# Kernel optimization log

Hardware: AMD Instinct MI355X
Metric: run time of the kernel (lower is better)

The kernel has to match this reference:

```python
import jax, jax.numpy as jnp
import numpy as np

NEG_INF = -1e8  # matches neg_inf in the torch source


def setup_inputs() -> dict:
    key = jax.random.key(0)
    k1, k2 = jax.random.split(key)
    N, M = 2048, 2048
    theta = jax.random.normal(k1, (N, M, 3), dtype=jnp.float32)
    A = jax.random.normal(k2, (3, 3), dtype=jnp.float32)
    return {"theta": theta, "A": A}


def _viterbi_forward(theta, A):
    # Softmax-smoothed Viterbi (Needleman-Wunsch-style) DP.
    # States: m=0, x=1, y=2.
    # V[i,j,m] = theta[i-1,j-1,m] + lse(V[i-1,j-1] + A[m])
    # V[i,j,x] = theta[i-1,j-1,x] + lse(V[i-1,j]   + A[x])
    # V[i,j,y] = theta[i-1,j-1,y] + lse(V[i,j-1]   + A[y])
    N, M, _ = theta.shape
    dt = theta.dtype
    ninf = jnp.asarray(NEG_INF, dt)
    Am, Ax, Ay = A[0], A[1], A[2]

    # Row 0 of V (columns 0..M): V[0,0]=[0,-inf,-inf], rest -inf.
    row0 = jnp.full((M + 1, 3), NEG_INF, dtype=dt).at[0, 0].set(0.0)

    def row_step(prev_row, theta_row):
        # prev_row: (M+1, 3) = V[i-1, 0..M]; theta_row: (M, 3) = theta[i-1]
        # m and x states depend only on the previous row -> vectorized over j.
        vm = jax.nn.logsumexp(prev_row[:-1] + Am, axis=-1) + theta_row[:, 0]  # (M,) j=1..M
        vx = jax.nn.logsumexp(prev_row[1:] + Ax, axis=-1) + theta_row[:, 1]   # (M,)
        # y state has a same-row recurrence over j -> scan over columns.
        vm_prev = jnp.concatenate([ninf[None], vm[:-1]])  # V[i, j-1, m]
        vx_prev = jnp.concatenate([ninf[None], vx[:-1]])  # V[i, j-1, x]

        def col_step(vy_prev, inputs):
            vmp, vxp, th_y = inputs
            vy = jax.nn.logsumexp(jnp.stack([vmp, vxp, vy_prev]) + Ay) + th_y
            return vy, vy

        _, vy = jax.lax.scan(col_step, ninf, (vm_prev, vx_prev, theta_row[:, 2]))
        new_row = jnp.concatenate(
            [jnp.full((1, 3), NEG_INF, dtype=dt),  # V[i, 0] = -inf
             jnp.stack([vm, vx, vy], axis=-1)], axis=0)
        return new_row, None

    last_row, _ = jax.lax.scan(row_step, row0, theta)
    # Terminal: Vt = lse(V[N, M])
    return jax.nn.logsumexp(last_row[M])


def reference(theta, A):
    return _viterbi_forward(theta, A)
```

## Files before the change

kernel.cpp:

```cpp
#include <hip/hip_runtime.h>

#define NDIM  2048
#define WAVES 32
#define BCOLS 2176
#define SLOTS 2128
#define ENCB  0x40000000
#define SENTV 0xFFFFFFFFFFFFFFFFull

typedef unsigned long long u64;

__device__ __align__(16) float4 g_S4[(size_t)WAVES * SLOTS * 64];
__device__ __align__(16) u64    g_B[(size_t)(WAVES+1) * BCOLS * 2];

__device__ __forceinline__ u64 ald(const u64* p) {
  return __hip_atomic_load(p, __ATOMIC_RELAXED, __HIP_MEMORY_SCOPE_AGENT);
}
__device__ __forceinline__ void ast(u64* p, u64 v) {
  __hip_atomic_store(p, v, __ATOMIC_RELAXED, __HIP_MEMORY_SCOPE_AGENT);
}
__device__ __forceinline__ float shup1(float x) {
  int v = __builtin_amdgcn_update_dpp(0, __float_as_int(x), 0x138, 0xf, 0xf, false);
  return __int_as_float(v);
}
__device__ __forceinline__ int imax(int a, int b) { return a > b ? a : b; }

__global__ void vit_prep_theta(const float* __restrict__ theta) {
  const int tid = blockIdx.x * blockDim.x + threadIdx.x;
  const int stride = gridDim.x * blockDim.x;
  const int total = WAVES * SLOTS * 64;
  for (int i = tid; i < total; i += stride) {
    const int l    = i & 63;
    const int rest = i >> 6;
    const int s    = rest % SLOTS;
    const int w    = rest / SLOTS;
    const int row  = w * 64 + l;
    const int col  = s - l;
    float4 r = make_float4(0.f, 0.f, 0.f, 0.f);
    if (col >= 0 && col < NDIM) {
      const float* tp = theta + ((size_t)row * NDIM + col) * 3;
      r.x = __expf(tp[0]); r.y = __expf(tp[1]); r.z = __expf(tp[2]);
    }
    g_S4[i] = r;
  }
}

__global__ void vit_prep_bnd() {
  const int tid = blockIdx.x * blockDim.x + threadIdx.x;
  const int stride = gridDim.x * blockDim.x;
  const int nb = (WAVES+1) * BCOLS;
  const u64 hi0 = ((u64)(unsigned)ENCB) << 32;
  for (int i = tid; i < nb; i += stride) {
    int w = i / BCOLS;
    int c = i - w * BCOLS;
    u64 lo, hi;
    if (c > NDIM)    { lo = 0ull; hi = hi0; }
    else if (w == 0) { lo = (c == 0) ? (u64)__float_as_uint(1.0f) : 0ull; hi = hi0; }
    else if (c == 0) { lo = 0ull; hi = hi0; }
    else             { lo = SENTV; hi = SENTV; }
    ast(&g_B[(size_t)i*2],   lo);
    ast(&g_B[(size_t)i*2+1], hi);
  }
}

__global__ void __launch_bounds__(64, 1)
__attribute__((amdgpu_waves_per_eu(1, 1)))
vit_main(const float* __restrict__ A, float* __restrict__ out) {
  const int lane = threadIdx.x;
  const int w    = blockIdx.x;
  const bool isL0 = (lane == 0);
  const int lsel = lane & 15;

  const float a00 = __expf(A[0]), a01 = __expf(A[1]), a02 = __expf(A[2]);
  const float a10 = __expf(A[3]), a11 = __expf(A[4]), a12 = __expf(A[5]);
  const float a20 = __expf(A[6]), a21 = __expf(A[7]), a22 = __expf(A[8]);

  const float4* tb4 = g_S4 + (size_t)w * SLOTS * 64 + lane;
  u64* bin  = g_B + (size_t)w     * BCOLS * 2;
  u64* bout = g_B + (size_t)(w+1) * BCOLS * 2;

  float Mp=0.f,Xp=0.f,Yp=0.f, Mu=0.f,Xu=0.f,Yu=0.f, Mud=0.f,Xud=0.f,Yud=0.f;
  int e_w = 0;

  float4 Ta0  = tb4[0*64],  Ta1  = tb4[1*64],  Ta2  = tb4[2*64],  Ta3  = tb4[3*64];
  float4 Ta4  = tb4[4*64],  Ta5  = tb4[5*64],  Ta6  = tb4[6*64],  Ta7  = tb4[7*64];
  float4 Ta8  = tb4[8*64],  Ta9  = tb4[9*64],  Ta10 = tb4[10*64], Ta11 = tb4[11*64];
  float4 Ta12 = tb4[12*64], Ta13 = tb4[13*64], Ta14 = tb4[14*64], Ta15 = tb4[15*64];
  float4 Tb0  = make_float4(0,0,0,0), Tb1  = Tb0, Tb2  = Tb0, Tb3  = Tb0;
  float4 Tb4  = Tb0, Tb5  = Tb0, Tb6  = Tb0, Tb7  = Tb0;
  float4 Tb8  = Tb0, Tb9  = Tb0, Tb10 = Tb0, Tb11 = Tb0;
  float4 Tb12 = Tb0, Tb13 = Tb0, Tb14 = Tb0, Tb15 = Tb0;

  u64 cLoa, cHia, cLob = 0, cHib = 0;
  u64* rpn;
  {
    u64* rp0 = bin + (size_t)(2 + lsel) * 2;
    cLoa = ald(rp0); cHia = ald(rp0 + 1);
    rpn = rp0 + 32;
  }

  {
    u64 lo = ald(bin), hi = ald(bin + 1);
    while (lo == SENTV || hi == SENTV) { __builtin_amdgcn_s_sleep(2); lo = ald(bin); hi = ald(bin+1); }
    if (isL0) {
      Mud = __uint_as_float((unsigned)lo);
      Xud = __uint_as_float((unsigned)(lo >> 32));
      Yud = __uint_as_float((unsigned)hi);
    }
  }
  {
    u64 lo = ald(bin + 2), hi = ald(bin + 3);
    while (lo == SENTV || hi == SENTV) { __builtin_amdgcn_s_sleep(8); lo = ald(bin+2); hi = ald(bin+3); }
    int ep = (int)((unsigned)(hi >> 32) - (unsigned)ENCB);
    int dd = ep - e_w;
    if (__builtin_amdgcn_readfirstlane(dd) > 48) { e_w = ep; dd = 0; }
    if (isL0) {
      Mu = ldexpf(__uint_as_float((unsigned)lo), dd);
      Xu = ldexpf(__uint_as_float((unsigned)(lo >> 32)), dd);
      Yu = ldexpf(__uint_as_float((unsigned)hi), dd);
    }
  }

#define STEP(U, S, SM, TM)                                                     \
  {                                                                            \
    const int s = base + (U) + 1;            \
    float mn = T##S##U.x * fmaf(a02, Yud, fmaf(a01, Xud, a00*Mud));            \
    float xn = T##S##U.y * fmaf(a12, Yu,  fmaf(a11, Xu,  a10*Mu));             \
    float yn = T##S##U.z * fmaf(a22, Yp,  fmaf(a21, Xp,  a20*Mp));             \
    if ((SM) ? (lane == 63) : (s >= 64 && lane == 63)) {                       \
      u64 slo = ((u64)__float_as_uint(xn) << 32) | __float_as_uint(mn);        \
      u64 shi = ((u64)(unsigned)(e_w + ENCB) << 32) | __float_as_uint(yn);     \
      ast(bO + (size_t)(U)*2,     slo);                                        \
      ast(bO + (size_t)(U)*2 + 1, shi);                                        \
    }                                                                          \
    if ((TM) && s == 2111 && w == 31 && lane == 63) {                          \
      out[0] = (log2f(mn + xn + yn) + (float)e_w) * 0.69314718055994531f;      \
    }                                                                          \
        \
    const float rM = __int_as_float(__builtin_amdgcn_readlane(__float_as_int(Mbf), (U))); \
    const float rX = __int_as_float(__builtin_amdgcn_readlane(__float_as_int(Xbf), (U))); \
    const float rY = __int_as_float(__builtin_amdgcn_readlane(__float_as_int(Ybf), (U))); \
                                                                   \
    Mud = Mu; Xud = Xu; Yud = Yu;                                              \
    const float sm = shup1(mn);                                                \
    const float sx = shup1(xn);                                                \
    const float sy = shup1(yn);                                                \
    Mu = isL0 ? rM : sm;                                                       \
    Xu = isL0 ? rX : sx;                                                       \
    Yu = isL0 ? rY : sy;                                                       \
    Mp = mn; Xp = xn; Yp = yn;                                                 \
  }

#define BLOCK(S, SN, SM, TM)                                                   \
  {                                                                            \
              \
    u64* rpc_ = rpn - 32;                                                      \
    bool bad_ = (cLo##S == SENTV) || (cHi##S == SENTV);                        \
    while (__ballot(bad_)) {                                                   \
      __builtin_amdgcn_s_sleep(1);                                             \
      cLo##S = ald(rpc_); cHi##S = ald(rpc_ + 1);                              \
      bad_ = (cLo##S == SENTV) || (cHi##S == SENTV);                           \
    }                                                                          \
                   \
    {                                                                          \
      const float4* tn_ = tb4 + (size_t)(base + 16) * 64;                      \
      T##SN##0  = tn_[0*64];  T##SN##1  = tn_[1*64];                           \
      T##SN##2  = tn_[2*64];  T##SN##3  = tn_[3*64];                           \
      T##SN##4  = tn_[4*64];  T##SN##5  = tn_[5*64];                           \
      T##SN##6  = tn_[6*64];  T##SN##7  = tn_[7*64];                           \
      T##SN##8  = tn_[8*64];  T##SN##9  = tn_[9*64];                           \
      T##SN##10 = tn_[10*64]; T##SN##11 = tn_[11*64];                          \
      T##SN##12 = tn_[12*64]; T##SN##13 = tn_[13*64];                          \
      T##SN##14 = tn_[14*64]; T##SN##15 = tn_[15*64];                          \
    }                                                                          \
    cLo##SN = ald(rpn); cHi##SN = ald(rpn + 1);                                \
    rpn += 32;                                                                 \
       \
    int dsl = ((int)(unsigned)(cHi##S >> 32) - ENCB) - e_w;                    \
    int dm = dsl;                                                              \
    dm = imax(dm, __shfl_xor(dm, 1));                                          \
    dm = imax(dm, __shfl_xor(dm, 2));                                          \
    dm = imax(dm, __shfl_xor(dm, 4));                                          \
    dm = imax(dm, __shfl_xor(dm, 8));       \
    if (dm > 0) {                                                              \
      const int sh = -dm;                                                      \
      Mp = ldexpf(Mp,sh); Xp = ldexpf(Xp,sh); Yp = ldexpf(Yp,sh);              \
      Mu = ldexpf(Mu,sh); Xu = ldexpf(Xu,sh); Yu = ldexpf(Yu,sh);              \
      Mud= ldexpf(Mud,sh);Xud= ldexpf(Xud,sh);Yud= ldexpf(Yud,sh);             \
      e_w += dm; dsl -= dm;                                                    \
    }                                                                          \
    const float Mbf = ldexpf(__uint_as_float((unsigned)cLo##S), dsl);          \
    const float Xbf = ldexpf(__uint_as_float((unsigned)(cLo##S >> 32)), dsl);  \
    const float Ybf = ldexpf(__uint_as_float((unsigned)cHi##S), dsl);          \
    __builtin_amdgcn_sched_barrier(0);                                         \
                                                       \
    u64* bO = bout + (size_t)(base - 62) * 2;                                  \
    STEP(0,S,SM,TM)  STEP(1,S,SM,TM)  STEP(2,S,SM,TM)  STEP(3,S,SM,TM)         \
    STEP(4,S,SM,TM)  STEP(5,S,SM,TM)  STEP(6,S,SM,TM)  STEP(7,S,SM,TM)         \
    STEP(8,S,SM,TM)  STEP(9,S,SM,TM)  STEP(10,S,SM,TM) STEP(11,S,SM,TM)        \
    STEP(12,S,SM,TM) STEP(13,S,SM,TM) STEP(14,S,SM,TM) STEP(15,S,SM,TM)        \
                 \
    {                                                                          \
      float m = fmaxf(fmaxf(Mp, Xp), Yp);                                      \
      const int jl = base + 16 - lane;                                         \
      if (jl < 1 || jl > NDIM) m = 0.0f;                                       \
      m = fmaxf(m, __shfl_xor(m, 1));                                          \
      m = fmaxf(m, __shfl_xor(m, 2));                                          \
      m = fmaxf(m, __shfl_xor(m, 4));                                          \
      m = fmaxf(m, __shfl_xor(m, 8));                                          \
      m = fmaxf(m, __shfl_xor(m, 16));                                         \
      m = fmaxf(m, __shfl_xor(m, 32));                                         \
      int E = (int)((__float_as_uint(m) >> 23) & 0xFF) - 127;                  \
      if (m == 0.0f) E = 0;                                                    \
      const int sh = -E;                                                       \
      Mp = ldexpf(Mp,sh); Xp = ldexpf(Xp,sh); Yp = ldexpf(Yp,sh);              \
      Mu = ldexpf(Mu,sh); Xu = ldexpf(Xu,sh); Yu = ldexpf(Yu,sh);              \
      Mud= ldexpf(Mud,sh);Xud= ldexpf(Xud,sh);Yud= ldexpf(Yud,sh);             \
      e_w += E;                                                                \
    }                                                                          \
    base += 16;                                                                \
  }

  int base = 0;
  BLOCK(a, b, 0, 0) BLOCK(b, a, 0, 0)
  BLOCK(a, b, 0, 0) BLOCK(b, a, 0, 0)
  for (int it = 0; it < 63; ++it) {
    BLOCK(a, b, 1, 0)
    BLOCK(b, a, 1, 0)
  }
  BLOCK(a, b, 1, 0)
  BLOCK(b, a, 1, 1)
#undef BLOCK
#undef STEP
}

extern "C" void kernel_launch(void* const* d_in, const int* in_sizes, int n_in,
                              void* d_out, int out_size, void* d_ws, size_t ws_size,
                              hipStream_t stream) {
  const float* theta = (const float*)d_in[0];
  const float* A     = (const float*)d_in[1];
  float* out = (float*)d_out;
  (void)in_sizes; (void)n_in; (void)out_size; (void)d_ws; (void)ws_size;
  vit_prep_theta<<<dim3(8192), dim3(256), 0, stream>>>(theta);
  vit_prep_bnd<<<dim3(256), dim3(256), 0, stream>>>();
  vit_main<<<dim3(WAVES), dim3(64), 0, stream>>>(A, out);
}
```

Baseline: 668.9 us.

## Stream theta through double-buffered LDS via global_load_lds and use DPP max reduction

Replaces the two register-resident 16-float4 theta prefetch buffers with a double-buffered LDS staging area filled by direct global-to-LDS loads, consuming it through a rolling window of four registers. This removes the a/b buffer alternation and about 128 VGPRs of prefetch state. The block loop becomes a single BLOCK macro. The per-block max reduction switches from ds_swizzle shuffles to DPP row/bcast ops plus a readlane, and the boundary exponent realignment is skipped when no lane needs it. The cost is LDS reads on the serial critical path and a waitcnt on every block.

```diff
diff --git a/kernel.cpp b/kernel.cpp
--- a/kernel.cpp
+++ b/kernel.cpp
@@ -22,7 +22,19 @@
   int v = __builtin_amdgcn_update_dpp(0, __float_as_int(x), 0x138, 0xf, 0xf, false);
   return __int_as_float(v);
 }
+template <int CTRL>
+__device__ __forceinline__ float maxdpp(float m) {
+  int v = __builtin_amdgcn_update_dpp(__float_as_int(m), __float_as_int(m),
+                                      CTRL, 0xf, 0xf, false);
+  return fmaxf(m, __int_as_float(v));
+}
 __device__ __forceinline__ int imax(int a, int b) { return a > b ? a : b; }
+
+typedef const __attribute__((address_space(1))) void GV;
+typedef __attribute__((address_space(3)))       void LV;
+__device__ __forceinline__ void gll16(const void* g, void* l) {
+  __builtin_amdgcn_global_load_lds((GV*)g, (LV*)l, 16, 0, 0);
+}
 
 __global__ void vit_prep_theta(const float* __restrict__ theta) {
   const int tid = blockIdx.x * blockDim.x + threadIdx.x;
@@ -65,6 +77,7 @@
 __global__ void __launch_bounds__(64, 1)
 __attribute__((amdgpu_waves_per_eu(1, 1)))
 vit_main(const float* __restrict__ A, float* __restrict__ out) {
+  __shared__ float4 sT[2048];
   const int lane = threadIdx.x;
   const int w    = blockIdx.x;
   const bool isL0 = (lane == 0);
@@ -81,22 +94,16 @@
   float Mp=0.f,Xp=0.f,Yp=0.f, Mu=0.f,Xu=0.f,Yu=0.f, Mud=0.f,Xud=0.f,Yud=0.f;
   int e_w = 0;
 
-  float4 Ta0  = tb4[0*64],  Ta1  = tb4[1*64],  Ta2  = tb4[2*64],  Ta3  = tb4[3*64];
-  float4 Ta4  = tb4[4*64],  Ta5  = tb4[5*64],  Ta6  = tb4[6*64],  Ta7  = tb4[7*64];
-  float4 Ta8  = tb4[8*64],  Ta9  = tb4[9*64],  Ta10 = tb4[10*64], Ta11 = tb4[11*64];
-  float4 Ta12 = tb4[12*64], Ta13 = tb4[13*64], Ta14 = tb4[14*64], Ta15 = tb4[15*64];
-  float4 Tb0  = make_float4(0,0,0,0), Tb1  = Tb0, Tb2  = Tb0, Tb3  = Tb0;
-  float4 Tb4  = Tb0, Tb5  = Tb0, Tb6  = Tb0, Tb7  = Tb0;
-  float4 Tb8  = Tb0, Tb9  = Tb0, Tb10 = Tb0, Tb11 = Tb0;
-  float4 Tb12 = Tb0, Tb13 = Tb0, Tb14 = Tb0, Tb15 = Tb0;
-
-  u64 cLoa, cHia, cLob = 0, cHib = 0;
   u64* rpn;
+  u64 cLo, cHi;
   {
     u64* rp0 = bin + (size_t)(2 + lsel) * 2;
-    cLoa = ald(rp0); cHia = ald(rp0 + 1);
+    cLo = ald(rp0); cHi = ald(rp0 + 1);
     rpn = rp0 + 32;
   }
+  #pragma unroll
+  for (int u_ = 0; u_ < 16; ++u_)
+    gll16(tb4 + (size_t)u_ * 64, &sT[u_ * 64]);
 
   {
     u64 lo = ald(bin), hi = ald(bin + 1);
@@ -120,12 +127,12 @@
     }
   }
 
-#define STEP(U, S, SM, TM)                                                     \
+#define STEPC(U, DV, SM, TM)                                                   \
   {                                                                            \
     const int s = base + (U) + 1;            \
-    float mn = T##S##U.x * fmaf(a02, Yud, fmaf(a01, Xud, a00*Mud));            \
-    float xn = T##S##U.y * fmaf(a12, Yu,  fmaf(a11, Xu,  a10*Mu));             \
-    float yn = T##S##U.z * fmaf(a22, Yp,  fmaf(a21, Xp,  a20*Mp));             \
+    float mn = DV.x * fmaf(a02, Yud, fmaf(a01, Xud, a00*Mud));                 \
+    float xn = DV.y * fmaf(a12, Yu,  fmaf(a11, Xu,  a10*Mu));                  \
+    float yn = DV.z * fmaf(a22, Yp,  fmaf(a21, Xp,  a20*Mp));                  \
     if ((SM) ? (lane == 63) : (s >= 64 && lane == 63)) {                       \
       u64 slo = ((u64)__float_as_uint(xn) << 32) | __float_as_uint(mn);        \
       u64 shi = ((u64)(unsigned)(e_w + ENCB) << 32) | __float_as_uint(yn);     \
@@ -149,88 +156,95 @@
     Yu = isL0 ? rY : sy;                                                       \
     Mp = mn; Xp = xn; Yp = yn;                                                 \
   }
-
-#define BLOCK(S, SN, SM, TM)                                                   \
+#define STEPR(U, DV, SM, TM) STEPC(U, DV, SM, TM) DV = sT[ldsA + ((U)+4)*64 + lane];
+
+#define BLOCK(SM, TM)                                                          \
   {                                                                            \
-              \
+    const unsigned ldsA = ((unsigned)(base >> 4) & 1u) << 10;                  \
+    const unsigned ldsB = ldsA ^ 1024u;                                        \
+            \
     u64* rpc_ = rpn - 32;                                                      \
-    bool bad_ = (cLo##S == SENTV) || (cHi##S == SENTV);                        \
+    bool bad_ = (cLo == SENTV) || (cHi == SENTV);                              \
     while (__ballot(bad_)) {                                                   \
       __builtin_amdgcn_s_sleep(1);                                             \
-      cLo##S = ald(rpc_); cHi##S = ald(rpc_ + 1);                              \
-      bad_ = (cLo##S == SENTV) || (cHi##S == SENTV);                           \
-    }                                                                          \
-                   \
+      cLo = ald(rpc_); cHi = ald(rpc_ + 1);                                    \
+      bad_ = (cLo == SENTV) || (cHi == SENTV);                                 \
+    }                                                                          \
+        \
+    __builtin_amdgcn_s_waitcnt(0x0F70);                     \
+    __builtin_amdgcn_sched_barrier(0);                                         \
+              \
+    u64 nLo = ald(rpn), nHi = ald(rpn + 1);                                    \
+    rpn += 32;                                                                 \
     {                                                                          \
       const float4* tn_ = tb4 + (size_t)(base + 16) * 64;                      \
-      T##SN##0  = tn_[0*64];  T##SN##1  = tn_[1*64];                           \
-      T##SN##2  = tn_[2*64];  T##SN##3  = tn_[3*64];                           \
-      T##SN##4  = tn_[4*64];  T##SN##5  = tn_[5*64];                           \
-      T##SN##6  = tn_[6*64];  T##SN##7  = tn_[7*64];                           \
-      T##SN##8  = tn_[8*64];  T##SN##9  = tn_[9*64];                           \
-      T##SN##10 = tn_[10*64]; T##SN##11 = tn_[11*64];                          \
-      T##SN##12 = tn_[12*64]; T##SN##13 = tn_[13*64];                          \
-      T##SN##14 = tn_[14*64]; T##SN##15 = tn_[15*64];                          \
-    }                                                                          \
-    cLo##SN = ald(rpn); cHi##SN = ald(rpn + 1);                                \
-    rpn += 32;                                                                 \
-       \
-    int dsl = ((int)(unsigned)(cHi##S >> 32) - ENCB) - e_w;                    \
-    int dm = dsl;                                                              \
-    dm = imax(dm, __shfl_xor(dm, 1));                                          \
-    dm = imax(dm, __shfl_xor(dm, 2));                                          \
-    dm = imax(dm, __shfl_xor(dm, 4));                                          \
-    dm = imax(dm, __shfl_xor(dm, 8));       \
-    if (dm > 0) {                                                              \
+      _Pragma("unroll")                                                        \
+      for (int u_ = 0; u_ < 16; ++u_)                                          \
+        gll16(tn_ + (size_t)u_ * 64, &sT[ldsB + u_ * 64]);                     \
+    }                                                                          \
+    __builtin_amdgcn_sched_barrier(0);                                         \
+             \
+    int dsl = ((int)(unsigned)(cHi >> 32) - ENCB) - e_w;                       \
+    if (__ballot(dsl > 0)) {                              \
+      int dm = dsl;                                                            \
+      dm = imax(dm, __shfl_xor(dm, 1));                                        \
+      dm = imax(dm, __shfl_xor(dm, 2));                                        \
+      dm = imax(dm, __shfl_xor(dm, 4));                                        \
+      dm = imax(dm, __shfl_xor(dm, 8));                                        \
       const int sh = -dm;                                                      \
       Mp = ldexpf(Mp,sh); Xp = ldexpf(Xp,sh); Yp = ldexpf(Yp,sh);              \
       Mu = ldexpf(Mu,sh); Xu = ldexpf(Xu,sh); Yu = ldexpf(Yu,sh);              \
       Mud= ldexpf(Mud,sh);Xud= ldexpf(Xud,sh);Yud= ldexpf(Yud,sh);             \
       e_w += dm; dsl -= dm;                                                    \
     }                                                                          \
-    const float Mbf = ldexpf(__uint_as_float((unsigned)cLo##S), dsl);          \
-    const float Xbf = ldexpf(__uint_as_float((unsigned)(cLo##S >> 32)), dsl);  \
-    const float Ybf = ldexpf(__uint_as_float((unsigned)cHi##S), dsl);          \
-    __builtin_amdgcn_sched_barrier(0);                                         \
+    const float Mbf = ldexpf(__uint_as_float((unsigned)cLo), dsl);             \
+    const float Xbf = ldexpf(__uint_as_float((unsigned)(cLo >> 32)), dsl);     \
+    const float Ybf = ldexpf(__uint_as_float((unsigned)cHi), dsl);             \
+                                \
+    float4 d0 = sT[ldsA + 0*64 + lane];                                        \
+    float4 d1 = sT[ldsA + 1*64 + lane];                                        \
+    float4 d2 = sT[ldsA + 2*64 + lane];                                        \
+    float4 d3 = sT[ldsA + 3*64 + lane];                                        \
                                                        \
     u64* bO = bout + (size_t)(base - 62) * 2;                                  \
-    STEP(0,S,SM,TM)  STEP(1,S,SM,TM)  STEP(2,S,SM,TM)  STEP(3,S,SM,TM)         \
-    STEP(4,S,SM,TM)  STEP(5,S,SM,TM)  STEP(6,S,SM,TM)  STEP(7,S,SM,TM)         \
-    STEP(8,S,SM,TM)  STEP(9,S,SM,TM)  STEP(10,S,SM,TM) STEP(11,S,SM,TM)        \
-    STEP(12,S,SM,TM) STEP(13,S,SM,TM) STEP(14,S,SM,TM) STEP(15,S,SM,TM)        \
-                 \
+    STEPR(0, d0, SM, TM)  STEPR(1, d1, SM, TM)                                 \
+    STEPR(2, d2, SM, TM)  STEPR(3, d3, SM, TM)                                 \
+    STEPR(4, d0, SM, TM)  STEPR(5, d1, SM, TM)                                 \
+    STEPR(6, d2, SM, TM)  STEPR(7, d3, SM, TM)                                 \
+    STEPR(8, d0, SM, TM)  STEPR(9, d1, SM, TM)                                 \
+    STEPR(10, d2, SM, TM) STEPR(11, d3, SM, TM)                                \
+    STEPC(12, d0, SM, TM) STEPC(13, d1, SM, TM)                                \
+    STEPC(14, d2, SM, TM) STEPC(15, d3, SM, TM)                                \
+                    \
     {                                                                          \
       float m = fmaxf(fmaxf(Mp, Xp), Yp);                                      \
       const int jl = base + 16 - lane;                                         \
       if (jl < 1 || jl > NDIM) m = 0.0f;                                       \
-      m = fmaxf(m, __shfl_xor(m, 1));                                          \
-      m = fmaxf(m, __shfl_xor(m, 2));                                          \
-      m = fmaxf(m, __shfl_xor(m, 4));                                          \
-      m = fmaxf(m, __shfl_xor(m, 8));                                          \
-      m = fmaxf(m, __shfl_xor(m, 16));                                         \
-      m = fmaxf(m, __shfl_xor(m, 32));                                         \
-      int E = (int)((__float_as_uint(m) >> 23) & 0xFF) - 127;                  \
-      if (m == 0.0f) E = 0;                                                    \
+      m = maxdpp<0x111>(m);                                    \
+      m = maxdpp<0x112>(m);                                    \
+      m = maxdpp<0x114>(m);                                    \
+      m = maxdpp<0x118>(m);                                    \
+      m = maxdpp<0x142>(m);                                  \
+      m = maxdpp<0x143>(m);            \
+      const int mb = __builtin_amdgcn_readlane(__float_as_int(m), 63);         \
+      int E = ((mb >> 23) & 0xFF) - 127;                                       \
+      if (mb == 0) E = 0;                                                      \
       const int sh = -E;                                                       \
       Mp = ldexpf(Mp,sh); Xp = ldexpf(Xp,sh); Yp = ldexpf(Yp,sh);              \
       Mu = ldexpf(Mu,sh); Xu = ldexpf(Xu,sh); Yu = ldexpf(Yu,sh);              \
       Mud= ldexpf(Mud,sh);Xud= ldexpf(Xud,sh);Yud= ldexpf(Yud,sh);             \
       e_w += E;                                                                \
     }                                                                          \
-    base += 16;                                                                \
+    base += 16; cLo = nLo; cHi = nHi;                                          \
   }
 
   int base = 0;
-  BLOCK(a, b, 0, 0) BLOCK(b, a, 0, 0)
-  BLOCK(a, b, 0, 0) BLOCK(b, a, 0, 0)
-  for (int it = 0; it < 63; ++it) {
-    BLOCK(a, b, 1, 0)
-    BLOCK(b, a, 1, 0)
-  }
-  BLOCK(a, b, 1, 0)
-  BLOCK(b, a, 1, 1)
+  BLOCK(0, 0) BLOCK(0, 0) BLOCK(0, 0) BLOCK(0, 0)
+  for (int it = 0; it < 127; ++it) { BLOCK(1, 0) }
+  BLOCK(1, 1)
 #undef BLOCK
-#undef STEP
+#undef STEPR
+#undef STEPC
 }
 
 extern "C" void kernel_launch(void* const* d_in, const int* in_sizes, int n_in,
```

After: 732.9 us. 9.6% more time.

## Batch boundary stores via LDS, check sentinels per word, use DPP max reduction

Applied to the files above, without the earlier changes.

The per-step boundary handoff is changed. Lane 63 no longer issues two global atomic stores on every step; it writes each step's result to shared memory, and after the 16-step block lanes 0-15 publish all 16 columns in parallel. The sentinel check now tests each 32-bit word, which guards against torn 64-bit reads, and the exponent-realignment shuffle reduction runs only when some lane needs it. The block-end max reduction uses DPP row operations plus a readlane instead of shfl_xor. Batching the stores removes serial store latency from the critical recurrence but delays publication to the downstream wave by up to a block.

```diff
diff --git a/kernel.cpp b/kernel.cpp
--- a/kernel.cpp
+++ b/kernel.cpp
@@ -21,6 +21,12 @@
 __device__ __forceinline__ float shup1(float x) {
   int v = __builtin_amdgcn_update_dpp(0, __float_as_int(x), 0x138, 0xf, 0xf, false);
   return __int_as_float(v);
+}
+template <int CTRL>
+__device__ __forceinline__ float maxdpp(float m) {
+  int v = __builtin_amdgcn_update_dpp(__float_as_int(m), __float_as_int(m),
+                                      CTRL, 0xf, 0xf, false);
+  return fmaxf(m, __int_as_float(v));
 }
 __device__ __forceinline__ int imax(int a, int b) { return a > b ? a : b; }
 
@@ -62,9 +68,15 @@
   }
 }
 
+__device__ __forceinline__ bool isbad(u64 lo, u64 hi) {
+  return ((unsigned)lo == 0xFFFFFFFFu) || ((unsigned)(lo >> 32) == 0xFFFFFFFFu) ||
+         ((unsigned)hi == 0xFFFFFFFFu) || ((unsigned)(hi >> 32) == 0xFFFFFFFFu);
+}
+
 __global__ void __launch_bounds__(64, 1)
 __attribute__((amdgpu_waves_per_eu(1, 1)))
 vit_main(const float* __restrict__ A, float* __restrict__ out) {
+  __shared__ float4 sB[16];
   const int lane = threadIdx.x;
   const int w    = blockIdx.x;
   const bool isL0 = (lane == 0);
@@ -100,7 +112,7 @@
 
   {
     u64 lo = ald(bin), hi = ald(bin + 1);
-    while (lo == SENTV || hi == SENTV) { __builtin_amdgcn_s_sleep(2); lo = ald(bin); hi = ald(bin+1); }
+    while (isbad(lo, hi)) { __builtin_amdgcn_s_sleep(2); lo = ald(bin); hi = ald(bin+1); }
     if (isL0) {
       Mud = __uint_as_float((unsigned)lo);
       Xud = __uint_as_float((unsigned)(lo >> 32));
@@ -109,7 +121,7 @@
   }
   {
     u64 lo = ald(bin + 2), hi = ald(bin + 3);
-    while (lo == SENTV || hi == SENTV) { __builtin_amdgcn_s_sleep(8); lo = ald(bin+2); hi = ald(bin+3); }
+    while (isbad(lo, hi)) { __builtin_amdgcn_s_sleep(8); lo = ald(bin+2); hi = ald(bin+3); }
     int ep = (int)((unsigned)(hi >> 32) - (unsigned)ENCB);
     int dd = ep - e_w;
     if (__builtin_amdgcn_readfirstlane(dd) > 48) { e_w = ep; dd = 0; }
@@ -120,18 +132,15 @@
     }
   }
 
-#define STEP(U, S, SM, TM)                                                     \
+#define STEP(U, S, TM)                                                         \
   {                                                                            \
     const int s = base + (U) + 1;            \
     float mn = T##S##U.x * fmaf(a02, Yud, fmaf(a01, Xud, a00*Mud));            \
     float xn = T##S##U.y * fmaf(a12, Yu,  fmaf(a11, Xu,  a10*Mu));             \
     float yn = T##S##U.z * fmaf(a22, Yp,  fmaf(a21, Xp,  a20*Mp));             \
-    if ((SM) ? (lane == 63) : (s >= 64 && lane == 63)) {                       \
-      u64 slo = ((u64)__float_as_uint(xn) << 32) | __float_as_uint(mn);        \
-      u64 shi = ((u64)(unsigned)(e_w + ENCB) << 32) | __float_as_uint(yn);     \
-      ast(bO + (size_t)(U)*2,     slo);                                        \
-      ast(bO + (size_t)(U)*2 + 1, shi);                                        \
-    }                                                                          \
+    \
+    if (lane == 63)                                                            \
+      sB[U] = make_float4(mn, xn, yn, __int_as_float(e_w + ENCB));             \
     if ((TM) && s == 2111 && w == 31 && lane == 63) {                          \
       out[0] = (log2f(mn + xn + yn) + (float)e_w) * 0.69314718055994531f;      \
     }                                                                          \
@@ -150,15 +159,15 @@
     Mp = mn; Xp = xn; Yp = yn;                                                 \
   }
 
-#define BLOCK(S, SN, SM, TM)                                                   \
+#define BLOCK(S, SN, TM)                                                       \
   {                                                                            \
               \
     u64* rpc_ = rpn - 32;                                                      \
-    bool bad_ = (cLo##S == SENTV) || (cHi##S == SENTV);                        \
+    bool bad_ = isbad(cLo##S, cHi##S);                                         \
     while (__ballot(bad_)) {                                                   \
       __builtin_amdgcn_s_sleep(1);                                             \
       cLo##S = ald(rpc_); cHi##S = ald(rpc_ + 1);                              \
-      bad_ = (cLo##S == SENTV) || (cHi##S == SENTV);                           \
+      bad_ = isbad(cLo##S, cHi##S);                                            \
     }                                                                          \
                    \
     {                                                                          \
@@ -174,14 +183,14 @@
     }                                                                          \
     cLo##SN = ald(rpn); cHi##SN = ald(rpn + 1);                                \
     rpn += 32;                                                                 \
-       \
+             \
     int dsl = ((int)(unsigned)(cHi##S >> 32) - ENCB) - e_w;                    \
-    int dm = dsl;                                                              \
-    dm = imax(dm, __shfl_xor(dm, 1));                                          \
-    dm = imax(dm, __shfl_xor(dm, 2));                                          \
-    dm = imax(dm, __shfl_xor(dm, 4));                                          \
-    dm = imax(dm, __shfl_xor(dm, 8));       \
-    if (dm > 0) {                                                              \
+    if (__ballot(dsl > 0)) {                              \
+      int dm = dsl;                                                            \
+      dm = imax(dm, __shfl_xor(dm, 1));                                        \
+      dm = imax(dm, __shfl_xor(dm, 2));                                        \
+      dm = imax(dm, __shfl_xor(dm, 4));                                        \
+      dm = imax(dm, __shfl_xor(dm, 8));                                        \
       const int sh = -dm;                                                      \
       Mp = ldexpf(Mp,sh); Xp = ldexpf(Xp,sh); Yp = ldexpf(Yp,sh);              \
       Mu = ldexpf(Mu,sh); Xu = ldexpf(Xu,sh); Yu = ldexpf(Yu,sh);              \
@@ -192,25 +201,37 @@
     const float Xbf = ldexpf(__uint_as_float((unsigned)(cLo##S >> 32)), dsl);  \
     const float Ybf = ldexpf(__uint_as_float((unsigned)cHi##S), dsl);          \
     __builtin_amdgcn_sched_barrier(0);                                         \
-                                                       \
-    u64* bO = bout + (size_t)(base - 62) * 2;                                  \
-    STEP(0,S,SM,TM)  STEP(1,S,SM,TM)  STEP(2,S,SM,TM)  STEP(3,S,SM,TM)         \
-    STEP(4,S,SM,TM)  STEP(5,S,SM,TM)  STEP(6,S,SM,TM)  STEP(7,S,SM,TM)         \
-    STEP(8,S,SM,TM)  STEP(9,S,SM,TM)  STEP(10,S,SM,TM) STEP(11,S,SM,TM)        \
-    STEP(12,S,SM,TM) STEP(13,S,SM,TM) STEP(14,S,SM,TM) STEP(15,S,SM,TM)        \
-                 \
+                             \
+    STEP(0,S,TM)  STEP(1,S,TM)  STEP(2,S,TM)  STEP(3,S,TM)                     \
+    STEP(4,S,TM)  STEP(5,S,TM)  STEP(6,S,TM)  STEP(7,S,TM)                     \
+    STEP(8,S,TM)  STEP(9,S,TM)  STEP(10,S,TM) STEP(11,S,TM)                    \
+    STEP(12,S,TM) STEP(13,S,TM) STEP(14,S,TM) STEP(15,S,TM)                    \
+        \
+    {                                                                          \
+      const int col_ = base - 62 + lane;                                       \
+      if (lane < 16 && col_ >= 1) {                                            \
+        float4 v = sB[lane];                                                   \
+        u64 lo_ = ((u64)__float_as_uint(v.y) << 32) | __float_as_uint(v.x);    \
+        u64 hi_ = ((u64)__float_as_uint(v.w) << 32) | __float_as_uint(v.z);    \
+        u64* bO_ = bout + (size_t)col_ * 2;                                    \
+        ast(bO_,     lo_);                                                     \
+        ast(bO_ + 1, hi_);                                                     \
+      }                                                                        \
+    }                                                                          \
+                    \
     {                                                                          \
       float m = fmaxf(fmaxf(Mp, Xp), Yp);                                      \
       const int jl = base + 16 - lane;                                         \
       if (jl < 1 || jl > NDIM) m = 0.0f;                                       \
-      m = fmaxf(m, __shfl_xor(m, 1));                                          \
-      m = fmaxf(m, __shfl_xor(m, 2));                                          \
-      m = fmaxf(m, __shfl_xor(m, 4));                                          \
-      m = fmaxf(m, __shfl_xor(m, 8));                                          \
-      m = fmaxf(m, __shfl_xor(m, 16));                                         \
-      m = fmaxf(m, __shfl_xor(m, 32));                                         \
-      int E = (int)((__float_as_uint(m) >> 23) & 0xFF) - 127;                  \
-      if (m == 0.0f) E = 0;                                                    \
+      m = maxdpp<0x111>(m);                                    \
+      m = maxdpp<0x112>(m);                                    \
+      m = maxdpp<0x114>(m);                                    \
+      m = maxdpp<0x118>(m);                                    \
+      m = maxdpp<0x142>(m);                                  \
+      m = maxdpp<0x143>(m);            \
+      const int mb = __builtin_amdgcn_readlane(__float_as_int(m), 63);         \
+      int E = ((mb >> 23) & 0xFF) - 127;                                       \
+      if (mb == 0) E = 0;                                                      \
       const int sh = -E;                                                       \
       Mp = ldexpf(Mp,sh); Xp = ldexpf(Xp,sh); Yp = ldexpf(Yp,sh);              \
       Mu = ldexpf(Mu,sh); Xu = ldexpf(Xu,sh); Yu = ldexpf(Yu,sh);              \
@@ -221,14 +242,13 @@
   }
 
   int base = 0;
-  BLOCK(a, b, 0, 0) BLOCK(b, a, 0, 0)
-  BLOCK(a, b, 0, 0) BLOCK(b, a, 0, 0)
-  for (int it = 0; it < 63; ++it) {
-    BLOCK(a, b, 1, 0)
-    BLOCK(b, a, 1, 0)
-  }
-  BLOCK(a, b, 1, 0)
-  BLOCK(b, a, 1, 1)
+  BLOCK(a, b, 0) BLOCK(b, a, 0)
+  for (int it = 0; it < 64; ++it) {
+    BLOCK(a, b, 0)
+    BLOCK(b, a, 0)
+  }
+  BLOCK(a, b, 0)
+  BLOCK(b, a, 1)
 #undef BLOCK
 #undef STEP
 }
```

Result: faster. 628.7 us (-6.0%).
